# Kernel optimization log

Hardware: AMD Instinct MI355X
Metric: run time of the kernel (lower is better)

Reference implementation:

```python
import math
import jax, jax.numpy as jnp
import numpy as np
from jax.scipy.special import xlogy, gammaln

HEADS = 8
DIM_KEY = 64
NUM_REL_POS_FEATURES = 192


def get_positional_embed(n, feature_size):
    # distances: [-n+1, ..., n-1], length 2n-1
    dist = jnp.arange(-n + 1, n)
    adist = jnp.abs(dist).astype(jnp.float32)[:, None]  # (2n-1, 1)
    num_basis = feature_size // 6  # 3 feature fns * 2 (sign-augmented)
    seq_len = n
    # exponential half-life features
    max_range = math.log(seq_len) / math.log(2.0)
    half_life = 2.0 ** jnp.linspace(3.0, max_range, num_basis)  # min_half_life=3.0
    feat_exp = jnp.exp(-math.log(2.0) / half_life[None, :] * adist)
    # central mask features
    center_widths = 2.0 ** jnp.arange(1, num_basis + 1) - 1.0
    feat_cm = (center_widths[None, :] > adist).astype(jnp.float32)
    # gamma pdf features
    stddev = seq_len / (2 * num_basis)
    start_mean = seq_len / num_basis
    mean = jnp.linspace(start_mean, float(seq_len), num_basis)[None, :]
    concentration = (mean / stddev) ** 2
    rate = mean / (stddev ** 2)
    log_unnorm = xlogy(concentration - 1.0, adist) - rate * adist
    log_norm = gammaln(concentration) - concentration * jnp.log(rate)
    prob = jnp.exp(log_unnorm - log_norm) + 1e-8
    feat_gamma = prob / jnp.max(prob, axis=-1, keepdims=True)
    emb = jnp.concatenate([feat_exp, feat_cm, feat_gamma], axis=-1)  # (2n-1, fs/2)
    sign = jnp.sign(dist).astype(jnp.float32)[:, None]
    return jnp.concatenate([emb, sign * emb], axis=-1)  # (2n-1, fs)


def relative_shift(x):
    # x: (b, h, n, 2n-1) -> (b, h, n, n) Transformer-XL shift
    b, h, t1, t2 = x.shape
    x = jnp.pad(x, ((0, 0), (0, 0), (0, 0), (1, 0)))  # (b,h,t1,t2+1)
    x = x.reshape(b, h, t2 + 1, t1)[:, :, 1:, :].reshape(b, h, t1, t2)
    return x[..., : (t2 + 2) // 2]


def setup_inputs() -> dict:
    key = jax.random.key(0)
    ks = jax.random.split(key, 8)
    dim = 1536
    b, n = 2, 1536
    hdk = HEADS * DIM_KEY  # 512
    hdv = HEADS * 192      # 1536
    s = 0.02
    return {
        'x': jax.random.normal(ks[0], (b, n, dim), jnp.float32),
        'Wq': jax.random.normal(ks[1], (hdk, dim), jnp.float32) * s,
        'Wk': jax.random.normal(ks[2], (hdk, dim), jnp.float32) * s,
        'Wv': jax.random.normal(ks[3], (hdv, dim), jnp.float32) * s,
        'Wrel': jax.random.normal(ks[4], (hdk, NUM_REL_POS_FEATURES), jnp.float32) * s,
        'Wout': jax.random.normal(ks[5], (dim, hdv), jnp.float32) * s,
        'b_out': jnp.zeros((dim,), jnp.float32),
        'rel_content_bias': jax.random.normal(ks[6], (1, HEADS, 1, DIM_KEY), jnp.float32),
        'rel_pos_bias': jax.random.normal(ks[7], (1, HEADS, 1, DIM_KEY), jnp.float32),
    }


def reference(x, Wq, Wk, Wv, Wrel, Wout, b_out, rel_content_bias, rel_pos_bias):
    b, n, dim = x.shape
    h = HEADS
    scale = DIM_KEY ** -0.5

    def split_heads(t):  # (b, n, h*d) -> (b, h, n, d)
        return t.reshape(b, n, h, -1).transpose(0, 2, 1, 3)

    q = split_heads(jnp.einsum('bnd,fd->bnf', x, Wq)) * scale
    k = split_heads(jnp.einsum('bnd,fd->bnf', x, Wk))
    v = split_heads(jnp.einsum('bnd,fd->bnf', x, Wv))

    content_logits = jnp.einsum('bhid,bhjd->bhij', q + rel_content_bias, k)

    positions = get_positional_embed(n, NUM_REL_POS_FEATURES)  # (2n-1, fs)
    rel_k = jnp.einsum('jf,ef->je', positions, Wrel).reshape(2 * n - 1, h, DIM_KEY)
    rel_k = rel_k.transpose(1, 0, 2)  # (h, 2n-1, dk)
    rel_logits = jnp.einsum('bhid,hjd->bhij', q + rel_pos_bias, rel_k)
    rel_logits = relative_shift(rel_logits)  # (b, h, n, n)

    attn = jax.nn.softmax(content_logits + rel_logits, axis=-1)
    out = jnp.einsum('bhij,bhjd->bhid', attn, v)
    out = out.transpose(0, 2, 1, 3).reshape(b, n, -1)  # (b, n, h*dv)
    return jnp.einsum('bnf,df->bnd', out, Wout) + b_out
```

## Files before the change

### kernel.cpp

```cpp
#include <hip/hip_runtime.h>
#include <cmath>

typedef unsigned short u16;
typedef unsigned int u32;
typedef short frag8 __attribute__((ext_vector_type(8)));
typedef float f32x4 __attribute__((ext_vector_type(4)));

#define DEVINL __device__ __forceinline__

DEVINL float bf2f(u16 v) { return __uint_as_float(((u32)v) << 16); }
DEVINL u16 f2bf(float f) {
    u32 u = __float_as_uint(f);
    u32 r = (u + 0x7fffu + ((u >> 16) & 1u)) >> 16;
    return (u16)r;
}
DEVINL u32 pack2(float a, float b) { return (u32)f2bf(a) | ((u32)f2bf(b) << 16); }
DEVINL void async_copy16(const u16* g, u16* l) {
    __builtin_amdgcn_global_load_lds((const __attribute__((address_space(1))) u32*)g,
                                     (__attribute__((address_space(3))) u32*)l, 16, 0, 0);
}
DEVINL f32x4 mfma_bf16(frag8 a, frag8 b, f32x4 c) {
    return __builtin_amdgcn_mfma_f32_16x16x32_bf16(a, b, c, 0, 0, 0);
}
#define VMCNT(N) asm volatile("s_waitcnt vmcnt(" #N ")" ::: "memory")
DEVINL void bar_raw() {
    asm volatile("s_waitcnt lgkmcnt(0)" ::: "memory");
    __builtin_amdgcn_s_barrier();
    asm volatile("" ::: "memory");
}

__global__ __launch_bounds__(256) void convert_kernel(
        const float* __restrict__ s0, const float* __restrict__ s1,
        const float* __restrict__ s2, const float* __restrict__ s3,
        const float* __restrict__ s4, u16* __restrict__ dst) {
    const int c0 = 589824, c1 = 98304, c2 = 98304, c3 = 294912;
    const int total = 1376256;
    for (int c = blockIdx.x * blockDim.x + threadIdx.x; c < total;
         c += gridDim.x * blockDim.x) {
        const float* src; int off;
        if (c < c0) { src = s0; off = c; }
        else if (c < c0 + c1) { src = s1; off = c - c0; }
        else if (c < c0 + c1 + c2) { src = s2; off = c - c0 - c1; }
        else if (c < c0 + c1 + c2 + c3) { src = s3; off = c - c0 - c1 - c2; }
        else { src = s4; off = c - c0 - c1 - c2 - c3; }
        float4 a = ((const float4*)src)[off * 2];
        float4 b = ((const float4*)src)[off * 2 + 1];
        uint4 o;
        o.x = pack2(a.x, a.y); o.y = pack2(a.z, a.w);
        o.z = pack2(b.x, b.y); o.w = pack2(b.z, b.w);
        ((uint4*)dst)[c] = o;
    }
}

DEVINL double lgamma_stirling(double z) {
    double zi = 1.0 / z, zi2 = zi * zi;
    return (z - 0.5) * log(z) - z + 0.91893853320467274178
         + zi * (1.0 / 12.0) - zi * zi2 * (1.0 / 360.0) + zi * zi2 * zi2 * (1.0 / 1260.0);
}

__global__ __launch_bounds__(256) void embed_relk_kernel(const float* __restrict__ Wrel,
                                                         u16* __restrict__ relk) {
    __shared__ float pos[16][192];
    __shared__ float inv_hl[32], cwid[32], cm1[32], rateS[32];
    __shared__ double lognS[32];
    __shared__ float gmax[16];
    int t = threadIdx.x;
    int u0b = blockIdx.x * 16;

    if (t < 32) {
        double step = (10.584962500721156 - 3.0) / 31.0;
        double hl = exp2(3.0 + t * step);
        inv_hl[t] = (float)(1.0 / hl);
        cwid[t] = exp2f((float)(t + 1)) - 1.0f;
        double mean = 48.0 * (t + 1);
        double conc = (mean / 24.0) * (mean / 24.0);
        double rate = mean / 576.0;
        cm1[t] = (float)(conc - 1.0);
        rateS[t] = (float)rate;
        lognS[t] = lgamma_stirling(conc) - conc * log(rate);
    }
    __syncthreads();

    for (int idx = t; idx < 512; idx += 256) {
        int ul = idx >> 5, bs = idx & 31;
        int dist = u0b + ul - 1535;
        float ad = fabsf((float)dist);
        pos[ul][bs] = exp2f(-ad * inv_hl[bs]);
        pos[ul][32 + bs] = (cwid[bs] > ad) ? 1.0f : 0.0f;
        double prob = 0.0;
        if (dist != 0) {
            double adD = (double)ad;
            prob = exp((double)cm1[bs] * log(adD) - (double)rateS[bs] * adD - lognS[bs]);
        }
        pos[ul][64 + bs] = (float)(prob + 1e-8);
    }
    __syncthreads();
    if (t < 16) {
        float g = 0.f;
        #pragma unroll
        for (int bsx = 0; bsx < 32; bsx++) g = fmaxf(g, pos[t][64 + bsx]);
        gmax[t] = g;
    }
    __syncthreads();
    for (int idx = t; idx < 16 * 96; idx += 256) {
        int ul = idx / 96, f = idx - ul * 96;
        float v = pos[ul][f];
        if (f >= 64) { v = v / gmax[ul]; pos[ul][f] = v; }
        int dist = u0b + ul - 1535;
        float sg = (dist > 0) ? 1.f : ((dist < 0) ? -1.f : 0.f);
        pos[ul][96 + f] = sg * v;
    }
    __syncthreads();

    int e0 = t * 2;
    const float* w0 = Wrel + e0 * 192;
    const float* w1 = w0 + 192;
    float a0[16], a1[16];
    #pragma unroll
    for (int ul = 0; ul < 16; ul++) { a0[ul] = 0.f; a1[ul] = 0.f; }
    for (int f = 0; f < 192; f++) {
        float wa = w0[f], wb = w1[f];
        #pragma unroll
        for (int ul = 0; ul < 16; ul++) {
            float p = pos[ul][f];
            a0[ul] = fmaf(p, wa, a0[ul]);
            a1[ul] = fmaf(p, wb, a1[ul]);
        }
    }
    int h0 = e0 >> 6, d0 = e0 & 63;
    int h1 = (e0 + 1) >> 6, d1 = (e0 + 1) & 63;
    for (int ul = 0; ul < 16; ul++) {
        int u = u0b + ul;
        relk[(h0 * 3072 + u) * 64 + d0] = f2bf(a0[ul]);
        relk[(h1 * 3072 + u) * 64 + d1] = f2bf(a1[ul]);
    }
}

DEVINL void gemm128_stage(const u16* __restrict__ A, const u16* __restrict__ B,
                          int K, int k0, u16* buf, int tid) {
    #pragma unroll
    for (int p = 0; p < 2; p++) {
        int e = (p * 256 + tid) * 8;
        int r = e >> 5, c = e & 31;
        async_copy16(A + r * K + k0 + c, buf + e);
        async_copy16(B + r * K + k0 + c, buf + 4096 + e);
    }
}

DEVINL void gemm128_mainloop(const u16* __restrict__ A, const u16* __restrict__ B,
                             int K, f32x4 acc[4][4], u16* smem) {
    int tid = threadIdx.x;
    int lane = tid & 63, wave = tid >> 6;
    int wm = (wave >> 1) * 64, wn = (wave & 1) * 64;
    int fm = lane & 15, fq = lane >> 4;
    const int NT = K >> 5;
    gemm128_stage(A, B, K, 0,  smem,         tid);
    gemm128_stage(A, B, K, 32, smem + 8192,  tid);
    gemm128_stage(A, B, K, 64, smem + 16384, tid);
    for (int t = 0; t < NT; t++) {
        u16* cur = smem + (t & 3) * 8192;
        if (t + 3 < NT) {
            gemm128_stage(A, B, K, (t + 3) * 32, smem + ((t + 3) & 3) * 8192, tid);
            VMCNT(12);
        } else if (t + 2 < NT) {
            VMCNT(8);
        } else if (t + 1 < NT) {
            VMCNT(4);
        } else {
            VMCNT(0);
        }
        bar_raw();
        frag8 af[4], bfr[4];
        #pragma unroll
        for (int mi = 0; mi < 4; mi++) af[mi] = *(const frag8*)&cur[(wm + 16 * mi + fm) * 32 + fq * 8];
        #pragma unroll
        for (int ni = 0; ni < 4; ni++) bfr[ni] = *(const frag8*)&cur[4096 + (wn + 16 * ni + fm) * 32 + fq * 8];
        #pragma unroll
        for (int mi = 0; mi < 4; mi++)
            #pragma unroll
            for (int ni = 0; ni < 4; ni++)
                acc[mi][ni] = mfma_bf16(af[mi], bfr[ni], acc[mi][ni]);
        bar_raw();
    }
}

__global__ __launch_bounds__(256) void gemm_qkv_kernel(
        const u16* __restrict__ X, const u16* __restrict__ Wq, const u16* __restrict__ Wk,
        const u16* __restrict__ Wv, const float* __restrict__ cbias, const float* __restrict__ pbias,
        u16* __restrict__ qc, u16* __restrict__ qp, u16* __restrict__ kws, u16* __restrict__ vt) {
    __shared__ __align__(16) u16 smem[32768];
    int m0 = blockIdx.x * 128, n0 = blockIdx.y * 128;
    const u16* Bp; int brow;
    if (n0 < 512)       { Bp = Wq; brow = n0; }
    else if (n0 < 1024) { Bp = Wk; brow = n0 - 512; }
    else                { Bp = Wv; brow = n0 - 1024; }
    f32x4 acc[4][4];
    #pragma unroll
    for (int i = 0; i < 4; i++)
        #pragma unroll
        for (int j = 0; j < 4; j++) acc[i][j] = (f32x4){0.f, 0.f, 0.f, 0.f};
    gemm128_mainloop(X + m0 * 1536, Bp + brow * 1536, 1536, acc, smem);

    int tid = threadIdx.x, lane = tid & 63, wave = tid >> 6;
    int wm = (wave >> 1) * 64, wn = (wave & 1) * 64, fm = lane & 15, fq = lane >> 4;
    #pragma unroll
    for (int mi = 0; mi < 4; mi++) {
        #pragma unroll
        for (int ni = 0; ni < 4; ni++) {
            int col = n0 + wn + 16 * ni + fm;
            int rbase = m0 + wm + 16 * mi + fq * 4;
            #pragma unroll
            for (int reg = 0; reg < 4; reg++) {
                int row = rbase + reg;
                float v = acc[mi][ni][reg];
                int b = row >= 1536 ? 1 : 0;
                int i = row - b * 1536;
                if (n0 < 512) {
                    float qv = v * 0.125f;
                    int idx = ((b * 8 + (col >> 6)) * 1536 + i) * 64 + (col & 63);
                    qc[idx] = f2bf(qv + cbias[col]);
                    qp[idx] = f2bf(qv + pbias[col]);
                } else if (n0 < 1024) {
                    int c2 = col - 512;
                    kws[((b * 8 + (c2 >> 6)) * 1536 + i) * 64 + (c2 & 63)] = f2bf(v);
                } else {
                    int c2 = col - 1024;
                    int hh = c2 / 192, dd = c2 - hh * 192;
                    vt[((b * 8 + hh) * 192 + dd) * 1536 + i] = f2bf(v);
                }
            }
        }
    }
}

DEVINL void stage_k(const u16* kP, u16* k_lds, int j0, int tid) {
    #pragma unroll
    for (int p = 0; p < 2; p++) {
        int l = p * 256 + tid, r = l >> 3, c = (l & 7) ^ (r & 7);
        async_copy16(kP + (j0 + r) * 64 + c * 8, k_lds + l * 8);
    }
}
DEVINL void stage_relk(const u16* rkP, u16* relk_lds, int u0, int tid) {
    #pragma unroll
    for (int p = 0; p < 3; p++) {
        int l = p * 256 + tid, r = l >> 3, c = (l & 7) ^ (r & 7);
        async_copy16(rkP + (u0 + r) * 64 + c * 8, relk_lds + l * 8);
    }
}

#define SP 68
#define RP 100

__global__ __launch_bounds__(256) void attn_kernel(
        const u16* __restrict__ qc, const u16* __restrict__ qp, const u16* __restrict__ kws,
        const u16* __restrict__ vt, const u16* __restrict__ relk, u16* __restrict__ ao) {
    __shared__ __align__(16) u16 smem[23232];
    u16* k_lds    = smem;
    u16* relk_lds = smem + 4096;
    u16* P_lds    = smem + 10240;
    float* S_lds  = (float*)(smem + 12288);
    float* R_lds  = (float*)(smem + 16640);
    float* mstate = (float*)(smem + 23040);
    float* lstate = mstate + 32;
    float* alpha_lds = lstate + 32;

    const int n = 1536;
    int flat = blockIdx.y * 48 + blockIdx.x;
    int swz  = (flat & 7) * 96 + (flat >> 3);
    int bh = swz / 48;
    int i0 = (swz - bh * 48) * 32;
    int b = bh >> 3, h = bh & 7;
    const u16* qcP = qc + bh * n * 64;
    const u16* qpP = qp + bh * n * 64;
    const u16* kP  = kws + bh * n * 64;
    const u16* vtP = vt + bh * 192 * n;
    const u16* rkP = relk + h * 3072 * 64;

    int tid = threadIdx.x, lane = tid & 63, w = tid >> 6, fm = lane & 15, fq = lane >> 4;
    int sw = fm & 7;
    if (tid < 32) { mstate[tid] = __int_as_float(0xff800000); lstate[tid] = 0.f; }

    frag8 aqc[2][2], aqp[2][2];
    #pragma unroll
    for (int mi = 0; mi < 2; mi++)
        #pragma unroll
        for (int ks = 0; ks < 2; ks++) {
            int off = (i0 + 16 * mi + fm) * 64 + ks * 32 + fq * 8;
            aqc[mi][ks] = *(const frag8*)(qcP + off);
            aqp[mi][ks] = *(const frag8*)(qpP + off);
        }

    f32x4 acc_o[2][3];
    #pragma unroll
    for (int mi = 0; mi < 2; mi++)
        #pragma unroll
        for (int dj = 0; dj < 3; dj++) acc_o[mi][dj] = (f32x4){0.f, 0.f, 0.f, 0.f};

    int uis[3], rmis[3];
    #pragma unroll
    for (int tt = 0; tt < 3; tt++) {
        int tv = w + tt * 4;
        rmis[tt] = (tv >= 6) ? 1 : 0;
        uis[tt] = tv - rmis[tt] * 6;
    }

    stage_k(kP, k_lds, 0, tid);
    stage_relk(rkP, relk_lds, 1504 - i0, tid);

    for (int jt = 0; jt < 24; jt++) {
        int j0 = jt * 64;
        VMCNT(0);
        bar_raw();

        frag8 fv[3][2];
        #pragma unroll
        for (int dj = 0; dj < 3; dj++)
            #pragma unroll
            for (int ks = 0; ks < 2; ks++)
                fv[dj][ks] = *(const frag8*)(vtP + (48 * w + 16 * dj + fm) * 1536
                                             + j0 + (4 * ks + fq) * 8);

        f32x4 acc_s[2];
        acc_s[0] = (f32x4){0.f, 0.f, 0.f, 0.f};
        acc_s[1] = (f32x4){0.f, 0.f, 0.f, 0.f};
        #pragma unroll
        for (int ks = 0; ks < 2; ks++) {
            frag8 bk = *(const frag8*)&k_lds[(16 * w + fm) * 64 + ((ks * 4 + fq) ^ sw) * 8];
            acc_s[0] = mfma_bf16(aqc[0][ks], bk, acc_s[0]);
            acc_s[1] = mfma_bf16(aqc[1][ks], bk, acc_s[1]);
        }
        f32x4 acc_r[3];
        #pragma unroll
        for (int tt = 0; tt < 3; tt++) {
            acc_r[tt] = (f32x4){0.f, 0.f, 0.f, 0.f};
            #pragma unroll
            for (int ks = 0; ks < 2; ks++) {
                frag8 br = *(const frag8*)&relk_lds[(16 * uis[tt] + fm) * 64 + ((ks * 4 + fq) ^ sw) * 8];
                acc_r[tt] = mfma_bf16(aqp[rmis[tt]][ks], br, acc_r[tt]);
            }
        }
        bar_raw();

        if (jt < 23) {
            stage_k(kP, k_lds, j0 + 64, tid);
            stage_relk(rkP, relk_lds, 1504 - i0 + j0 + 64, tid);
        }

        #pragma unroll
        for (int mi = 0; mi < 2; mi++)
            #pragma unroll
            for (int reg = 0; reg < 4; reg++)
                S_lds[(16 * mi + fq * 4 + reg) * SP + 16 * w + fm] = acc_s[mi][reg];
        #pragma unroll
        for (int tt = 0; tt < 3; tt++)
            #pragma unroll
            for (int reg = 0; reg < 4; reg++)
                R_lds[(16 * rmis[tt] + fq * 4 + reg) * RP + 16 * uis[tt] + fm] = acc_r[tt][reg];
        bar_raw();

        int li = tid >> 3, c0 = (tid & 7) * 8;
        float sv[8];
        {
            float4 sa = *(const float4*)(S_lds + li * SP + c0);
            float4 sb = *(const float4*)(S_lds + li * SP + c0 + 4);
            sv[0] = sa.x; sv[1] = sa.y; sv[2] = sa.z; sv[3] = sa.w;
            sv[4] = sb.x; sv[5] = sb.y; sv[6] = sb.z; sv[7] = sb.w;
        }
        const float* rrow = R_lds + li * RP + c0 - li + 31;
        float mx = __int_as_float(0xff800000);
        #pragma unroll
        for (int e = 0; e < 8; e++) {
            sv[e] += rrow[e];
            mx = fmaxf(mx, sv[e]);
        }
        mx = fmaxf(mx, __shfl_xor(mx, 1));
        mx = fmaxf(mx, __shfl_xor(mx, 2));
        mx = fmaxf(mx, __shfl_xor(mx, 4));
        float mo = mstate[li];
        float mn = fmaxf(mo, mx);
        float al = __expf(mo - mn);
        float pe[8], sum = 0.f;
        #pragma unroll
        for (int e = 0; e < 8; e++) { pe[e] = __expf(sv[e] - mn); sum += pe[e]; }
        {
            uint4 pw;
            pw.x = pack2(pe[0], pe[1]); pw.y = pack2(pe[2], pe[3]);
            pw.z = pack2(pe[4], pe[5]); pw.w = pack2(pe[6], pe[7]);
            int slot = (tid & 7) ^ (li & 7);
            *(uint4*)&P_lds[li * 64 + slot * 8] = pw;
        }
        sum += __shfl_xor(sum, 1);
        sum += __shfl_xor(sum, 2);
        sum += __shfl_xor(sum, 4);
        if ((tid & 7) == 0) {
            mstate[li] = mn;
            lstate[li] = lstate[li] * al + sum;
            alpha_lds[li] = al;
        }
        bar_raw();

        #pragma unroll
        for (int mi = 0; mi < 2; mi++)
            #pragma unroll
            for (int reg = 0; reg < 4; reg++) {
                float al2 = alpha_lds[16 * mi + fq * 4 + reg];
                #pragma unroll
                for (int dj = 0; dj < 3; dj++) acc_o[mi][dj][reg] *= al2;
            }
        frag8 ap[2][2];
        #pragma unroll
        for (int mi = 0; mi < 2; mi++)
            #pragma unroll
            for (int ks = 0; ks < 2; ks++)
                ap[mi][ks] = *(const frag8*)&P_lds[(16 * mi + fm) * 64 + ((ks * 4 + fq) ^ sw) * 8];
        #pragma unroll
        for (int dj = 0; dj < 3; dj++) {
            #pragma unroll
            for (int ks = 0; ks < 2; ks++) {
                acc_o[0][dj] = mfma_bf16(ap[0][ks], fv[dj][ks], acc_o[0][dj]);
                acc_o[1][dj] = mfma_bf16(ap[1][ks], fv[dj][ks], acc_o[1][dj]);
            }
        }
    }

    #pragma unroll
    for (int mi = 0; mi < 2; mi++)
        #pragma unroll
        for (int dj = 0; dj < 3; dj++)
            #pragma unroll
            for (int reg = 0; reg < 4; reg++) {
                int rl = 16 * mi + fq * 4 + reg;
                float lsum = lstate[rl];
                int row = b * 1536 + i0 + rl;
                int col = h * 192 + 16 * (3 * w + dj) + fm;
                ao[row * 1536 + col] = f2bf(acc_o[mi][dj][reg] / lsum);
            }
}

__global__ __launch_bounds__(256) void gemm_out_kernel(
        const u16* __restrict__ A, const u16* __restrict__ W, const float* __restrict__ bias,
        float* __restrict__ out) {
    __shared__ __align__(16) u16 smem[32768];
    int m0 = blockIdx.x * 128, n0 = blockIdx.y * 128;
    f32x4 acc[4][4];
    #pragma unroll
    for (int i = 0; i < 4; i++)
        #pragma unroll
        for (int j = 0; j < 4; j++) acc[i][j] = (f32x4){0.f, 0.f, 0.f, 0.f};
    gemm128_mainloop(A + m0 * 1536, W + n0 * 1536, 1536, acc, smem);

    int tid = threadIdx.x, lane = tid & 63, wave = tid >> 6;
    int wm = (wave >> 1) * 64, wn = (wave & 1) * 64, fm = lane & 15, fq = lane >> 4;
    #pragma unroll
    for (int mi = 0; mi < 4; mi++) {
        #pragma unroll
        for (int ni = 0; ni < 4; ni++) {
            int col = n0 + wn + 16 * ni + fm;
            int rbase = m0 + wm + 16 * mi + fq * 4;
            float bv = bias[col];
            #pragma unroll
            for (int reg = 0; reg < 4; reg++) {
                int row = rbase + reg;
                out[row * 1536 + col] = acc[mi][ni][reg] + bv;
            }
        }
    }
}

extern "C" void kernel_launch(void* const* d_in, const int* in_sizes, int n_in,
                              void* d_out, int out_size, void* d_ws, size_t ws_size,
                              hipStream_t stream) {
    (void)in_sizes; (void)n_in; (void)out_size; (void)ws_size;
    const float* x    = (const float*)d_in[0];
    const float* Wq   = (const float*)d_in[1];
    const float* Wk   = (const float*)d_in[2];
    const float* Wv   = (const float*)d_in[3];
    const float* Wrel = (const float*)d_in[4];
    const float* Wout = (const float*)d_in[5];
    const float* bout = (const float*)d_in[6];
    const float* cb   = (const float*)d_in[7];
    const float* pb   = (const float*)d_in[8];

    u16* xb  = (u16*)d_ws;
    u16* wqb = xb  + 4718592;
    u16* wkb = wqb + 786432;
    u16* wvb = wkb + 786432;
    u16* wob = wvb + 2359296;
    u16* qc  = wob + 2359296;
    u16* qp  = qc + 1572864;
    u16* kw  = qp + 1572864;
    u16* vt  = kw + 1572864;
    u16* rk  = vt + 4718592;
    u16* ao  = rk + 1572864;
    float* out = (float*)d_out;

    convert_kernel<<<dim3(1024), dim3(256), 0, stream>>>(x, Wq, Wk, Wv, Wout, xb);
    embed_relk_kernel<<<dim3(192), dim3(256), 0, stream>>>(Wrel, rk);
    gemm_qkv_kernel<<<dim3(24, 20), dim3(256), 0, stream>>>(xb, wqb, wkb, wvb, cb, pb, qc, qp, kw, vt);
    attn_kernel<<<dim3(48, 16), dim3(256), 0, stream>>>(qc, qp, kw, vt, rk, ao);
    gemm_out_kernel<<<dim3(24, 12), dim3(256), 0, stream>>>(ao, wob, bout, out);
}
```

Before: 315.2 us.

## Load K and rel-K fragments directly into registers, drop LDS staging

```diff
diff --git a/kernel.cpp b/kernel.cpp
--- a/kernel.cpp
+++ b/kernel.cpp
@@ -233,34 +233,17 @@
     }
 }
 
-DEVINL void stage_k(const u16* kP, u16* k_lds, int j0, int tid) {
-    #pragma unroll
-    for (int p = 0; p < 2; p++) {
-        int l = p * 256 + tid, r = l >> 3, c = (l & 7) ^ (r & 7);
-        async_copy16(kP + (j0 + r) * 64 + c * 8, k_lds + l * 8);
-    }
-}
-DEVINL void stage_relk(const u16* rkP, u16* relk_lds, int u0, int tid) {
-    #pragma unroll
-    for (int p = 0; p < 3; p++) {
-        int l = p * 256 + tid, r = l >> 3, c = (l & 7) ^ (r & 7);
-        async_copy16(rkP + (u0 + r) * 64 + c * 8, relk_lds + l * 8);
-    }
-}
-
 #define SP 68
 #define RP 100
 
 __global__ __launch_bounds__(256) void attn_kernel(
         const u16* __restrict__ qc, const u16* __restrict__ qp, const u16* __restrict__ kws,
         const u16* __restrict__ vt, const u16* __restrict__ relk, u16* __restrict__ ao) {
-    __shared__ __align__(16) u16 smem[23232];
-    u16* k_lds    = smem;
-    u16* relk_lds = smem + 4096;
-    u16* P_lds    = smem + 10240;
-    float* S_lds  = (float*)(smem + 12288);
-    float* R_lds  = (float*)(smem + 16640);
-    float* mstate = (float*)(smem + 23040);
+    __shared__ __align__(16) u16 smem[12992];
+    u16* P_lds    = smem;
+    float* S_lds  = (float*)(smem + 2048);
+    float* R_lds  = (float*)(smem + 6400);
+    float* mstate = (float*)(smem + 12800);
     float* lstate = mstate + 32;
     float* alpha_lds = lstate + 32;
 
@@ -304,46 +287,52 @@
         uis[tt] = tv - rmis[tt] * 6;
     }
 
-    stage_k(kP, k_lds, 0, tid);
-    stage_relk(rkP, relk_lds, 1504 - i0, tid);
+    const u16* kIt = kP + (16 * w + fm) * 64 + fq * 8;
+    const u16* rIt0 = rkP + (1504 - i0 + 16 * uis[0] + fm) * 64 + fq * 8;
+    const u16* rIt1 = rkP + (1504 - i0 + 16 * uis[1] + fm) * 64 + fq * 8;
+    const u16* rIt2 = rkP + (1504 - i0 + 16 * uis[2] + fm) * 64 + fq * 8;
+    const u16* vBase = vtP + (48 * w + fm) * 1536 + fq * 8;
+
+    frag8 fk[2], fr0[2], fr1[2], fr2[2];
+    fk[0]  = *(const frag8*)(kIt);       fk[1]  = *(const frag8*)(kIt + 32);
+    fr0[0] = *(const frag8*)(rIt0);      fr0[1] = *(const frag8*)(rIt0 + 32);
+    fr1[0] = *(const frag8*)(rIt1);      fr1[1] = *(const frag8*)(rIt1 + 32);
+    fr2[0] = *(const frag8*)(rIt2);      fr2[1] = *(const frag8*)(rIt2 + 32);
+    kIt += 4096; rIt0 += 4096; rIt1 += 4096; rIt2 += 4096;
 
     for (int jt = 0; jt < 24; jt++) {
         int j0 = jt * 64;
-        VMCNT(0);
-        bar_raw();
-
         frag8 fv[3][2];
         #pragma unroll
         for (int dj = 0; dj < 3; dj++)
             #pragma unroll
             for (int ks = 0; ks < 2; ks++)
-                fv[dj][ks] = *(const frag8*)(vtP + (48 * w + 16 * dj + fm) * 1536
-                                             + j0 + (4 * ks + fq) * 8);
+                fv[dj][ks] = *(const frag8*)(vBase + dj * 16 * 1536 + j0 + ks * 32);
 
         f32x4 acc_s[2];
         acc_s[0] = (f32x4){0.f, 0.f, 0.f, 0.f};
         acc_s[1] = (f32x4){0.f, 0.f, 0.f, 0.f};
         #pragma unroll
         for (int ks = 0; ks < 2; ks++) {
-            frag8 bk = *(const frag8*)&k_lds[(16 * w + fm) * 64 + ((ks * 4 + fq) ^ sw) * 8];
-            acc_s[0] = mfma_bf16(aqc[0][ks], bk, acc_s[0]);
-            acc_s[1] = mfma_bf16(aqc[1][ks], bk, acc_s[1]);
+            acc_s[0] = mfma_bf16(aqc[0][ks], fk[ks], acc_s[0]);
+            acc_s[1] = mfma_bf16(aqc[1][ks], fk[ks], acc_s[1]);
         }
         f32x4 acc_r[3];
         #pragma unroll
-        for (int tt = 0; tt < 3; tt++) {
-            acc_r[tt] = (f32x4){0.f, 0.f, 0.f, 0.f};
-            #pragma unroll
-            for (int ks = 0; ks < 2; ks++) {
-                frag8 br = *(const frag8*)&relk_lds[(16 * uis[tt] + fm) * 64 + ((ks * 4 + fq) ^ sw) * 8];
-                acc_r[tt] = mfma_bf16(aqp[rmis[tt]][ks], br, acc_r[tt]);
-            }
-        }
-        bar_raw();
+        for (int tt = 0; tt < 3; tt++) acc_r[tt] = (f32x4){0.f, 0.f, 0.f, 0.f};
+        #pragma unroll
+        for (int ks = 0; ks < 2; ks++) {
+            acc_r[0] = mfma_bf16(aqp[rmis[0]][ks], fr0[ks], acc_r[0]);
+            acc_r[1] = mfma_bf16(aqp[rmis[1]][ks], fr1[ks], acc_r[1]);
+            acc_r[2] = mfma_bf16(aqp[rmis[2]][ks], fr2[ks], acc_r[2]);
+        }
 
         if (jt < 23) {
-            stage_k(kP, k_lds, j0 + 64, tid);
-            stage_relk(rkP, relk_lds, 1504 - i0 + j0 + 64, tid);
+            fk[0]  = *(const frag8*)(kIt);   fk[1]  = *(const frag8*)(kIt + 32);
+            fr0[0] = *(const frag8*)(rIt0);  fr0[1] = *(const frag8*)(rIt0 + 32);
+            fr1[0] = *(const frag8*)(rIt1);  fr1[1] = *(const frag8*)(rIt1 + 32);
+            fr2[0] = *(const frag8*)(rIt2);  fr2[1] = *(const frag8*)(rIt2 + 32);
+            kIt += 4096; rIt0 += 4096; rIt1 += 4096; rIt2 += 4096;
         }
 
         #pragma unroll
```

Measured after the change: 329.3 us. +4.5%, slower.
